# Optimization experiments

Measured on AMD Instinct MI355X. Metric: run time of the kernel, lower is better.

The kernel has to match this reference:

```python
import jax, jax.numpy as jnp
import numpy as np

MU = 0.5
SIGMA = 0.5


def relu_zono(M, c, slopes):
    """Zonotope ReLU relaxation with learnable slopes.
    M: [k, n] error-term magnitudes, c: [n] center, slopes: [n].
    Returns (M', c') where M' has n extra rows (new error terms; rows for
    non-crossing neurons are exactly zero, matching the torch math up to
    zero-row padding so shapes stay static under jit).
    """
    abs_vals = jnp.sum(jnp.abs(M), axis=0)            # [n]
    lx = c - abs_vals
    ux = c + abs_vals
    basic = ux / (ux - lx)                            # denom = 2*abs_vals > 0 a.s.
    zero_mask = ux <= 0
    cross_mask = (ux > 0) & (lx <= 0)
    in_range = (slopes >= 0) & (slopes <= basic)
    left = cross_mask & in_range
    right = cross_mask & jnp.logical_not(in_range)
    mag = jnp.where(left, (1.0 - slopes) * ux * 0.5,
          jnp.where(right, -slopes * lx * 0.5, 0.0))  # [n] new error magnitudes
    col_scale = jnp.where(zero_mask, 0.0, jnp.where(cross_mask, slopes, 1.0))
    M = M * col_scale[None, :]
    c = jnp.where(zero_mask, 0.0, jnp.where(cross_mask, slopes * c + mag, c))
    M = jnp.concatenate([M, jnp.diag(mag)], axis=0)   # one new row per neuron
    return M, c


def zono_forward(M, c, slopes1, slopes2, W1, b1, W2, b2, W3, b3):
    # Normalization layer: center normalized, magnitudes divided by sigma
    c = (c - MU) / SIGMA
    M = M / SIGMA
    # Linear 1 (bias only applies to center, matching F.linear(M, W) w/o bias)
    M = M @ W1.T
    c = c @ W1.T + b1
    M, c = relu_zono(M, c, slopes1)
    # Linear 2
    M = M @ W2.T
    c = c @ W2.T + b2
    M, c = relu_zono(M, c, slopes2)
    # Linear 3 (logits)
    M = M @ W3.T
    c = c @ W3.T + b3
    return M, c


def setup_inputs() -> dict:
    key = jax.random.key(0)
    ks = jax.random.split(key, 10)
    d_in, h, d_out = 3072, 4096, 10
    magnitude_matrix = jax.random.normal(ks[0], (d_in, d_in), jnp.float32) * 0.001
    center = jax.random.normal(ks[1], (d_in,), jnp.float32)
    slopes1 = jax.random.uniform(ks[2], (h,), jnp.float32)
    slopes2 = jax.random.uniform(ks[3], (h,), jnp.float32)
    W1 = jax.random.normal(ks[4], (h, d_in), jnp.float32) / np.sqrt(d_in)
    b1 = jax.random.normal(ks[5], (h,), jnp.float32) * 0.1
    W2 = jax.random.normal(ks[6], (h, h), jnp.float32) / np.sqrt(h)
    b2 = jax.random.normal(ks[7], (h,), jnp.float32) * 0.1
    W3 = jax.random.normal(ks[8], (d_out, h), jnp.float32) / np.sqrt(h)
    b3 = jax.random.normal(ks[9], (d_out,), jnp.float32) * 0.1
    return {"magnitude_matrix": magnitude_matrix, "center": center,
            "slopes1": slopes1, "slopes2": slopes2,
            "W1": W1, "b1": b1, "W2": W2, "b2": b2, "W3": W3, "b3": b3}


def reference(magnitude_matrix, center, slopes1, slopes2, W1, b1, W2, b2, W3, b3):
    return zono_forward(magnitude_matrix, center, slopes1, slopes2,
                        W1, b1, W2, b2, W3, b3)
```

## Files before the change

kernel.cpp:

```cpp
#include <hip/hip_runtime.h>
#include <cstddef>
#include <cstdint>

#define DIN 3072
#define DH  4096
#define DOUT 10

typedef float4 f4;
typedef __attribute__((ext_vector_type(4))) int   int32x4;
typedef __attribute__((ext_vector_type(8))) char  charx8;

#define R_A1 0.013f
#define R_W1 0.117275f
#define R_T1 0.013f
#define R_W2 0.1015625f

__device__ __forceinline__ short f2bf(float x) {
    unsigned u = __builtin_bit_cast(unsigned, x);
    u = (u + 0x7FFFu + ((u >> 16) & 1u)) >> 16;
    return (short)u;
}
__device__ __forceinline__ float bf2f(short x) {
    unsigned u = ((unsigned)(unsigned short)x) << 16;
    return __builtin_bit_cast(float, u);
}
__device__ __forceinline__ char q8(float x, float s) {
    float r = rintf(x * s);
    r = fminf(127.f, fmaxf(-127.f, r));
    return (char)(int)r;
}

__device__ __forceinline__ void gload_lds16(const char* g, char* l) {
    __builtin_amdgcn_global_load_lds(
        (const __attribute__((address_space(1))) unsigned int*)g,
        (__attribute__((address_space(3))) unsigned int*)l,
        16, 0, 0);
}

__global__ void init_kernel(const float* __restrict__ c, float* __restrict__ cn,
                            float* __restrict__ abs1, float* __restrict__ out) {
    int i = blockIdx.x * 256 + threadIdx.x;
    abs1[i] = 0.f;
    if (i < DIN) cn[i] = (c[i] - 0.5f) * 2.0f;
    size_t base = (size_t)(DIN + i) * DOUT;
#pragma unroll
    for (int o = 0; o < DOUT; ++o) out[base + o] = 0.f;
}

__global__ void quant8_kernel(const float* __restrict__ in, char* __restrict__ out,
                              float s, int n8) {
    int i = blockIdx.x * 256 + threadIdx.x;
    if (i >= n8) return;
    const f4* p = (const f4*)(in + (size_t)i * 8);
    f4 v0 = p[0], v1 = p[1];
    charx8 o;
    o[0] = q8(v0.x, s); o[1] = q8(v0.y, s); o[2] = q8(v0.z, s); o[3] = q8(v0.w, s);
    o[4] = q8(v1.x, s); o[5] = q8(v1.y, s); o[6] = q8(v1.z, s); o[7] = q8(v1.w, s);
    *(charx8*)(out + (size_t)i * 8) = o;
}

__global__ __launch_bounds__(384)
void quant_w1_fused(const float* __restrict__ W1, const float* __restrict__ cn,
                    char* __restrict__ W1q, float* __restrict__ c1acc, float s)
{
    int j = blockIdx.x, t = threadIdx.x;
    int lane = t & 63, wave = t >> 6;
    const float* row = W1 + (size_t)j * DIN;
    size_t base = (size_t)t * 8;
    f4 v0 = *(const f4*)&row[base], v1 = *(const f4*)&row[base + 4];
    f4 u0 = *(const f4*)&cn[base],  u1 = *(const f4*)&cn[base + 4];
    charx8 o;
    o[0] = q8(v0.x, s); o[1] = q8(v0.y, s); o[2] = q8(v0.z, s); o[3] = q8(v0.w, s);
    o[4] = q8(v1.x, s); o[5] = q8(v1.y, s); o[6] = q8(v1.z, s); o[7] = q8(v1.w, s);
    *(charx8*)&W1q[(size_t)j * DIN + base] = o;
    float acc = v0.x*u0.x + v0.y*u0.y + v0.z*u0.z + v0.w*u0.w
              + v1.x*u1.x + v1.y*u1.y + v1.z*u1.z + v1.w*u1.w;
#pragma unroll
    for (int m = 32; m >= 1; m >>= 1) acc += __shfl_xor(acc, m, 64);
    __shared__ float red[6];
    if (lane == 0) red[wave] = acc;
    __syncthreads();
    if (t == 0) c1acc[j] = red[0] + red[1] + red[2] + red[3] + red[4] + red[5];
}

__global__ __launch_bounds__(512)
void quant_w2_fused(const float* __restrict__ W2, const float* __restrict__ cs1,
                    const float* __restrict__ c1p, const float* __restrict__ mag1,
                    char* __restrict__ W2q, float* __restrict__ c2acc,
                    float* __restrict__ abs2, float s)
{
    int j = blockIdx.x, t = threadIdx.x;
    int lane = t & 63, wave = t >> 6;
    const float* row = W2 + (size_t)j * DH;
    size_t base = (size_t)t * 8;
    f4 v0 = *(const f4*)&row[base], v1 = *(const f4*)&row[base + 4];
    f4 s0 = *(const f4*)&cs1[base], s1 = *(const f4*)&cs1[base + 4];
    f4 p0 = *(const f4*)&c1p[base], p1 = *(const f4*)&c1p[base + 4];
    f4 m0 = *(const f4*)&mag1[base], m1 = *(const f4*)&mag1[base + 4];
    charx8 o;
    o[0] = q8(v0.x * s0.x, s); o[1] = q8(v0.y * s0.y, s);
    o[2] = q8(v0.z * s0.z, s); o[3] = q8(v0.w * s0.w, s);
    o[4] = q8(v1.x * s1.x, s); o[5] = q8(v1.y * s1.y, s);
    o[6] = q8(v1.z * s1.z, s); o[7] = q8(v1.w * s1.w, s);
    *(charx8*)&W2q[(size_t)j * DH + base] = o;
    float a = p0.x*v0.x + p0.y*v0.y + p0.z*v0.z + p0.w*v0.w
            + p1.x*v1.x + p1.y*v1.y + p1.z*v1.z + p1.w*v1.w;
    float b = m0.x*fabsf(v0.x) + m0.y*fabsf(v0.y) + m0.z*fabsf(v0.z) + m0.w*fabsf(v0.w)
            + m1.x*fabsf(v1.x) + m1.y*fabsf(v1.y) + m1.z*fabsf(v1.z) + m1.w*fabsf(v1.w);
#pragma unroll
    for (int m = 32; m >= 1; m >>= 1) {
        a += __shfl_xor(a, m, 64);
        b += __shfl_xor(b, m, 64);
    }
    __shared__ float reda[8], redb[8];
    if (lane == 0) { reda[wave] = a; redb[wave] = b; }
    __syncthreads();
    if (t == 0) {
        float sa = 0.f, sb = 0.f;
#pragma unroll
        for (int w = 0; w < 8; ++w) { sa += reda[w]; sb += redb[w]; }
        c2acc[j] = sa; abs2[j] = sb;
    }
}

template<int OUT8>
__global__ __launch_bounds__(512, 2)
void gemm_i8nt(const char* __restrict__ A, const char* __restrict__ B,
               void* __restrict__ Cout, float* __restrict__ absout,
               int M, int N, int K, float ds, float oscale)
{
    __shared__ char lds[2][4][16384];

    const int tid  = threadIdx.x;
    const int lane = tid & 63, wid = tid >> 6;
    const int wm = wid >> 2, wn = wid & 3;
    const int fr = lane & 15, fh = lane >> 4;

    const int gx = gridDim.x;
    const int nwg = gx * gridDim.y;
    const int orig = blockIdx.y * gx + blockIdx.x;
    const int swz = (orig & 7) * (nwg >> 3) + (orig >> 3);
    const int bx = swz % gx, by = swz / gx;
    const int row0 = by * 256, col0 = bx * 256;

    const char* Apan = A + (size_t)row0 * K;
    const char* Bpan = B + (size_t)col0 * K;

    const int s0 = wid * 64 + lane;
    const int r0 = s0 >> 3;  const int c0 = ((s0 & 7) ^ (r0 & 7)) * 16;
    const int s1 = s0 + 512;
    const int r1 = s1 >> 3;  const int c1 = ((s1 & 7) ^ (r1 & 7)) * 16;
    const int d0 = wid * 1024;
    const int d1 = 8192 + wid * 1024;

    const int xr = fr & 7;
    const int ch0 = ((0 + fh) ^ xr) * 16;
    const int ch1 = ((4 + fh) ^ xr) * 16;
    const int brow = (wn & 1) * 64;

#define STAGE(bi, part, u) do {                                                   \
    const char* _s = ((part) < 2 ? Apan : Bpan)                                   \
                     + (size_t)(((part) & 1) * 128) * K + (size_t)(u) * 128;      \
    char* _d = &lds[bi][part][0];                                                 \
    gload_lds16(_s + (size_t)r0 * K + c0, _d + d0);                               \
    gload_lds16(_s + (size_t)r1 * K + c1, _d + d1);                               \
} while (0)

    int32x4 acc[8][4];
#pragma unroll
    for (int i = 0; i < 8; ++i)
#pragma unroll
        for (int j = 0; j < 4; ++j) acc[i][j] = (int32x4){0, 0, 0, 0};

    int32x4 a[4][2], b0[2][2], b1[2][2];
    const int NT = K >> 7;

#define KSTEP(CUR, NXT, SA, AU, SB, BU, LAST)                                      \
  {                                                                                \
    const char* Al = &lds[CUR][wm][0];                                             \
    const char* Bl = &lds[CUR][2 + (wn >> 1)][0];                                  \
                                                                \
    _Pragma("unroll") for (int f = 0; f < 4; ++f) {                                \
      a[f][0] = *(const int32x4*)&Al[(f * 16 + fr) * 128 + ch0];                   \
      a[f][1] = *(const int32x4*)&Al[(f * 16 + fr) * 128 + ch1];                   \
    }                                                                              \
    _Pragma("unroll") for (int nf = 0; nf < 2; ++nf) {                             \
      b0[nf][0] = *(const int32x4*)&Bl[(brow + nf * 16 + fr) * 128 + ch0];         \
      b0[nf][1] = *(const int32x4*)&Bl[(brow + nf * 16 + fr) * 128 + ch1];         \
    }                                                                              \
    if (SA) STAGE(NXT, 0, AU);                                                     \
    __builtin_amdgcn_s_barrier();                                                  \
    asm volatile("s_waitcnt lgkmcnt(0)" ::: "memory");                             \
    __builtin_amdgcn_sched_barrier(0);                                             \
    __builtin_amdgcn_s_setprio(1);                                                 \
    _Pragma("unroll") for (int f = 0; f < 4; ++f)                                  \
      _Pragma("unroll") for (int nf = 0; nf < 2; ++nf) {                           \
        acc[f][nf] = __builtin_amdgcn_mfma_i32_16x16x64_i8(a[f][0], b0[nf][0], acc[f][nf], 0, 0, 0); \
        acc[f][nf] = __builtin_amdgcn_mfma_i32_16x16x64_i8(a[f][1], b0[nf][1], acc[f][nf], 0, 0, 0); \
      }                                                                            \
    __builtin_amdgcn_s_setprio(0);                                                 \
    __builtin_amdgcn_s_barrier();                                                  \
                                                                \
    _Pragma("unroll") for (int nf = 0; nf < 2; ++nf) {                             \
      b1[nf][0] = *(const int32x4*)&Bl[(brow + 32 + nf * 16 + fr) * 128 + ch0];    \
      b1[nf][1] = *(const int32x4*)&Bl[(brow + 32 + nf * 16 + fr) * 128 + ch1];    \
    }                                                                              \
    if (SA) STAGE(NXT, 1, AU);                                                     \
    __builtin_amdgcn_s_barrier();                                                  \
    asm volatile("s_waitcnt lgkmcnt(0)" ::: "memory");                             \
    __builtin_amdgcn_sched_barrier(0);                                             \
    __builtin_amdgcn_s_setprio(1);                                                 \
    _Pragma("unroll") for (int f = 0; f < 4; ++f)                                  \
      _Pragma("unroll") for (int nf = 0; nf < 2; ++nf) {                           \
        acc[f][2+nf] = __builtin_amdgcn_mfma_i32_16x16x64_i8(a[f][0], b1[nf][0], acc[f][2+nf], 0, 0, 0); \
        acc[f][2+nf] = __builtin_amdgcn_mfma_i32_16x16x64_i8(a[f][1], b1[nf][1], acc[f][2+nf], 0, 0, 0); \
      }                                                                            \
    __builtin_amdgcn_s_setprio(0);                                                 \
    __builtin_amdgcn_s_barrier();                                                  \
                                                                \
    _Pragma("unroll") for (int f = 0; f < 4; ++f) {                                \
      a[f][0] = *(const int32x4*)&Al[((f + 4) * 16 + fr) * 128 + ch0];             \
      a[f][1] = *(const int32x4*)&Al[((f + 4) * 16 + fr) * 128 + ch1];             \
    }                                                                              \
    if (SB) STAGE(CUR, 2, BU);                                                     \
    __builtin_amdgcn_s_barrier();                                                  \
    asm volatile("s_waitcnt lgkmcnt(0)" ::: "memory");                             \
    __builtin_amdgcn_sched_barrier(0);                                             \
    __builtin_amdgcn_s_setprio(1);                                                 \
    _Pragma("unroll") for (int f = 0; f < 4; ++f)                                  \
      _Pragma("unroll") for (int nf = 0; nf < 2; ++nf) {                           \
        acc[4+f][2+nf] = __builtin_amdgcn_mfma_i32_16x16x64_i8(a[f][0], b1[nf][0], acc[4+f][2+nf], 0, 0, 0); \
        acc[4+f][2+nf] = __builtin_amdgcn_mfma_i32_16x16x64_i8(a[f][1], b1[nf][1], acc[4+f][2+nf], 0, 0, 0); \
      }                                                                            \
    __builtin_amdgcn_s_setprio(0);                                                 \
    __builtin_amdgcn_s_barrier();                                                  \
                                                 \
    if (SB) STAGE(CUR, 3, BU);                                                     \
    __builtin_amdgcn_s_setprio(1);                                                 \
    _Pragma("unroll") for (int f = 0; f < 4; ++f)                                  \
      _Pragma("unroll") for (int nf = 0; nf < 2; ++nf) {                           \
        acc[4+f][nf] = __builtin_amdgcn_mfma_i32_16x16x64_i8(a[f][0], b0[nf][0], acc[4+f][nf], 0, 0, 0); \
        acc[4+f][nf] = __builtin_amdgcn_mfma_i32_16x16x64_i8(a[f][1], b0[nf][1], acc[4+f][nf], 0, 0, 0); \
      }                                                                            \
    __builtin_amdgcn_s_setprio(0);                                                 \
    if (LAST) { asm volatile("s_waitcnt vmcnt(0)" ::: "memory"); }                 \
    else      { asm volatile("s_waitcnt vmcnt(4)" ::: "memory"); }                 \
    __builtin_amdgcn_s_barrier();                                                  \
  }

    STAGE(0, 0, 0); STAGE(0, 1, 0); STAGE(0, 2, 0); STAGE(0, 3, 0);
    STAGE(1, 2, 1); STAGE(1, 3, 1);
    asm volatile("s_waitcnt vmcnt(4)" ::: "memory");
    __builtin_amdgcn_s_barrier();

    int u = 0;
    for (; u + 3 < NT; u += 2) {
        KSTEP(0, 1, 1, u + 1, 1, u + 2, 0)
        KSTEP(1, 0, 1, u + 2, 1, u + 3, 0)
    }
    KSTEP(0, 1, 1, NT - 1, 0, 0, 1)
    KSTEP(1, 0, 0, 0, 0, 0, 1)
#undef KSTEP
#undef STAGE

    const int cr = row0 + wm * 128 + fh * 4;
    const int cc = col0 + wn * 64 + fr;
    float csum[4];
#pragma unroll
    for (int nf = 0; nf < 4; ++nf) {
        float s = 0.f;
#pragma unroll
        for (int f = 0; f < 8; ++f)
#pragma unroll
            for (int j = 0; j < 4; ++j) {
                float v = (float)acc[f][nf][j] * ds;
                s += fabsf(v);
                size_t idx = (size_t)(cr + f * 16 + j) * N + cc + nf * 16;
                if (OUT8) ((char*)Cout)[idx] = q8(v, oscale);
                else      ((short*)Cout)[idx] = f2bf(v);
            }
        s += __shfl_xor(s, 16, 64);
        s += __shfl_xor(s, 32, 64);
        csum[nf] = s;
    }
    if (fh == 0) {
#pragma unroll
        for (int nf = 0; nf < 4; ++nf)
            atomicAdd(&absout[col0 + wn * 64 + nf * 16 + fr], csum[nf]);
    }
}

__global__ void relu_params_kernel(const float* __restrict__ absv, const float* __restrict__ cacc,
                                   const float* __restrict__ bias, const float* __restrict__ slopes,
                                   float* __restrict__ mag, float* __restrict__ cs,
                                   float* __restrict__ cp, int n)
{
    int j = blockIdx.x * 256 + threadIdx.x;
    if (j >= n) return;
    float a = absv[j];
    float cin = cacc[j] + bias[j];
    float s = slopes[j];
    float lx = cin - a, ux = cin + a;
    float basic = ux / (ux - lx);
    bool zero  = (ux <= 0.f);
    bool cross = (ux > 0.f) && (lx <= 0.f);
    bool inr   = (s >= 0.f) && (s <= basic);
    float mg = cross ? (inr ? (1.f - s) * ux * 0.5f : -s * lx * 0.5f) : 0.f;
    mag[j] = mg;
    cs[j]  = zero ? 0.f : (cross ? s : 1.f);
    cp[j]  = zero ? 0.f : (cross ? s * cin + mg : cin);
}

__global__ void relu2_fused(const float* __restrict__ absv, const float* __restrict__ cacc,
                            const float* __restrict__ bias, const float* __restrict__ slopes,
                            const float* __restrict__ W3,
                            float* __restrict__ cp, float* __restrict__ V,
                            float* __restrict__ out)
{
    int j = blockIdx.x * 256 + threadIdx.x;
    if (j >= DH) return;
    float a = absv[j];
    float cin = cacc[j] + bias[j];
    float s = slopes[j];
    float lx = cin - a, ux = cin + a;
    float basic = ux / (ux - lx);
    bool zero  = (ux <= 0.f);
    bool cross = (ux > 0.f) && (lx <= 0.f);
    bool inr   = (s >= 0.f) && (s <= basic);
    float mg = cross ? (inr ? (1.f - s) * ux * 0.5f : -s * lx * 0.5f) : 0.f;
    float csv = zero ? 0.f : (cross ? s : 1.f);
    cp[j] = zero ? 0.f : (cross ? s * cin + mg : cin);
    size_t base = (size_t)(DIN + DH + j) * DOUT;
#pragma unroll
    for (int o = 0; o < DOUT; ++o) {
        float w = W3[(size_t)o * DH + j];
        V[j * DOUT + o] = csv * w;
        out[base + o] = mg * w;
    }
}

__global__ __launch_bounds__(256)
void out_fused(const short* __restrict__ T2, const float* __restrict__ V,
               const float* __restrict__ W2, const float* __restrict__ mag1,
               const float* __restrict__ c2p, const float* __restrict__ W3,
               const float* __restrict__ b3, float* __restrict__ out)
{
    int b = blockIdx.x, tid = threadIdx.x;
    int lane = tid & 63, wave = tid >> 6;
    __shared__ float red[4][DOUT];

    if (b < DIN / 4) {
        int r = b * 4 + wave;
        const short* trow = T2 + (size_t)r * DH;
        float acc[DOUT];
#pragma unroll
        for (int o = 0; o < DOUT; ++o) acc[o] = 0.f;
        for (int j = lane; j < DH; j += 64) {
            float t = bf2f(trow[j]);
            const float* vr = V + j * DOUT;
#pragma unroll
            for (int o = 0; o < DOUT; ++o) acc[o] += t * vr[o];
        }
#pragma unroll
        for (int o = 0; o < DOUT; ++o)
            for (int m = 32; m >= 1; m >>= 1) acc[o] += __shfl_xor(acc[o], m, 64);
        if (lane == 0) {
#pragma unroll
            for (int o = 0; o < DOUT; ++o) out[(size_t)r * DOUT + o] = acc[o];
        }
    } else if (b < DIN / 4 + 256) {
        int bb = b - DIN / 4;
        int i = (bb & 15) * 256 + tid;
        int j0 = (bb >> 4) * 256;
        float acc[DOUT];
#pragma unroll
        for (int o = 0; o < DOUT; ++o) acc[o] = 0.f;
        for (int j = j0; j < j0 + 256; ++j) {
            float w = W2[(size_t)j * DH + i];
            const float* vr = V + j * DOUT;
#pragma unroll
            for (int o = 0; o < DOUT; ++o) acc[o] += w * vr[o];
        }
        float m = mag1[i];
        size_t base = (size_t)(DIN + i) * DOUT;
#pragma unroll
        for (int o = 0; o < DOUT; ++o) atomicAdd(&out[base + o], m * acc[o]);
    } else {
        float acc[DOUT];
#pragma unroll
        for (int o = 0; o < DOUT; ++o) acc[o] = 0.f;
        for (int j = tid; j < DH; j += 256) {
            float cv = c2p[j];
#pragma unroll
            for (int o = 0; o < DOUT; ++o) acc[o] += cv * W3[(size_t)o * DH + j];
        }
#pragma unroll
        for (int o = 0; o < DOUT; ++o)
            for (int m = 32; m >= 1; m >>= 1) acc[o] += __shfl_xor(acc[o], m, 64);
        if (lane == 0)
#pragma unroll
            for (int o = 0; o < DOUT; ++o) red[wave][o] = acc[o];
        __syncthreads();
        if (tid < DOUT) {
            float s = red[0][tid] + red[1][tid] + red[2][tid] + red[3][tid] + b3[tid];
            out[(size_t)(DIN + DH + DH) * DOUT + tid] = s;
        }
    }
}

extern "C" void kernel_launch(void* const* d_in, const int* in_sizes, int n_in,
                              void* d_out, int out_size, void* d_ws, size_t ws_size,
                              hipStream_t stream)
{
    const float* Mm = (const float*)d_in[0];
    const float* c  = (const float*)d_in[1];
    const float* s1 = (const float*)d_in[2];
    const float* s2 = (const float*)d_in[3];
    const float* W1 = (const float*)d_in[4];
    const float* b1 = (const float*)d_in[5];
    const float* W2 = (const float*)d_in[6];
    const float* b2 = (const float*)d_in[7];
    const float* W3 = (const float*)d_in[8];
    const float* b3 = (const float*)d_in[9];
    float* out = (float*)d_out;

    char* w = (char*)d_ws;
    short* T2b  = (short*)w;                                  w += (size_t)DIN * DH * 2;
    float* V    = (float*)w;                                  w += (size_t)DH * DOUT * 4;
    float* abs1 = (float*)w;                                  w += DH * 4;
    float* abs2 = (float*)w;                                  w += DH * 4;
    float* mag1 = (float*)w;                                  w += DH * 4;
    float* cs1  = (float*)w;                                  w += DH * 4;
    float* c1p  = (float*)w;                                  w += DH * 4;
    float* c1acc= (float*)w;                                  w += DH * 4;
    float* c2acc= (float*)w;                                  w += DH * 4;
    float* c2p  = (float*)w;                                  w += DH * 4;
    float* cn   = (float*)w;                                  w += DIN * 4;
    char*  Aq   = w;                                          w += (size_t)DIN * DIN;
    char*  Wq   = w;                                          w += (size_t)DH * DH;
    char*  T1q  = w;                                          w += (size_t)DIN * DH;

    const float invA1 = 127.f / R_A1;
    const float invW1 = 127.f / R_W1;
    const float invT1 = 127.f / R_T1;
    const float invW2 = 127.f / R_W2;
    const float ds1 = (R_A1 / 127.f) * (R_W1 / 127.f);
    const float ds2 = (R_T1 / 127.f) * (R_W2 / 127.f);

    init_kernel<<<16, 256, 0, stream>>>(c, cn, abs1, out);

    quant8_kernel<<<DIN * DIN / 8 / 256, 256, 0, stream>>>(Mm, Aq, 2.f * invA1, DIN * DIN / 8);
    quant_w1_fused<<<DH, 384, 0, stream>>>(W1, cn, Wq, c1acc, invW1);

    gemm_i8nt<1><<<dim3(DH / 256, DIN / 256), 512, 0, stream>>>(
        Aq, Wq, T1q, abs1, DIN, DH, DIN, ds1, invT1);
    relu_params_kernel<<<16, 256, 0, stream>>>(abs1, c1acc, b1, s1, mag1, cs1, c1p, DH);

    quant_w2_fused<<<DH, 512, 0, stream>>>(W2, cs1, c1p, mag1, Wq, c2acc, abs2, invW2);
    gemm_i8nt<0><<<dim3(DH / 256, DIN / 256), 512, 0, stream>>>(
        T1q, Wq, T2b, abs2, DIN, DH, DH, ds2, 0.f);
    relu2_fused<<<16, 256, 0, stream>>>(abs2, c2acc, b2, s2, W3, c2p, V, out);

    out_fused<<<DIN / 4 + 256 + 1, 256, 0, stream>>>(T2b, V, W2, mag1, c2p, W3, b3, out);
}
```

Before: 203.1 us.

## Fuse prep kernels, use 192-row GEMM tiles, read int8 W2 in output stage

Merges the init, A-quantisation and W1-quantisation kernels into one launch and folds the centre normalisation into the W1 dot product. Both int8 GEMMs switch from 256x256 to 192x256 tiles, which gives 16x16=256 workgroups instead of 192 and so fills more CUs, at the cost of less reuse per tile. The final stage now reads the already quantised, slope-scaled int8 W2 with a per-column correction factor instead of the fp32 W2, cutting its memory traffic but adding a division by the column scale.

```diff
diff --git a/kernel.cpp b/kernel.cpp
--- a/kernel.cpp
+++ b/kernel.cpp
@@ -37,50 +37,52 @@
         16, 0, 0);
 }
 
-__global__ void init_kernel(const float* __restrict__ c, float* __restrict__ cn,
-                            float* __restrict__ abs1, float* __restrict__ out) {
-    int i = blockIdx.x * 256 + threadIdx.x;
-    abs1[i] = 0.f;
-    if (i < DIN) cn[i] = (c[i] - 0.5f) * 2.0f;
-    size_t base = (size_t)(DIN + i) * DOUT;
-#pragma unroll
-    for (int o = 0; o < DOUT; ++o) out[base + o] = 0.f;
-}
-
-__global__ void quant8_kernel(const float* __restrict__ in, char* __restrict__ out,
-                              float s, int n8) {
-    int i = blockIdx.x * 256 + threadIdx.x;
-    if (i >= n8) return;
-    const f4* p = (const f4*)(in + (size_t)i * 8);
-    f4 v0 = p[0], v1 = p[1];
-    charx8 o;
-    o[0] = q8(v0.x, s); o[1] = q8(v0.y, s); o[2] = q8(v0.z, s); o[3] = q8(v0.w, s);
-    o[4] = q8(v1.x, s); o[5] = q8(v1.y, s); o[6] = q8(v1.z, s); o[7] = q8(v1.w, s);
-    *(charx8*)(out + (size_t)i * 8) = o;
-}
-
 __global__ __launch_bounds__(384)
-void quant_w1_fused(const float* __restrict__ W1, const float* __restrict__ cn,
-                    char* __restrict__ W1q, float* __restrict__ c1acc, float s)
-{
-    int j = blockIdx.x, t = threadIdx.x;
-    int lane = t & 63, wave = t >> 6;
-    const float* row = W1 + (size_t)j * DIN;
-    size_t base = (size_t)t * 8;
-    f4 v0 = *(const f4*)&row[base], v1 = *(const f4*)&row[base + 4];
-    f4 u0 = *(const f4*)&cn[base],  u1 = *(const f4*)&cn[base + 4];
-    charx8 o;
-    o[0] = q8(v0.x, s); o[1] = q8(v0.y, s); o[2] = q8(v0.z, s); o[3] = q8(v0.w, s);
-    o[4] = q8(v1.x, s); o[5] = q8(v1.y, s); o[6] = q8(v1.z, s); o[7] = q8(v1.w, s);
-    *(charx8*)&W1q[(size_t)j * DIN + base] = o;
-    float acc = v0.x*u0.x + v0.y*u0.y + v0.z*u0.z + v0.w*u0.w
-              + v1.x*u1.x + v1.y*u1.y + v1.z*u1.z + v1.w*u1.w;
-#pragma unroll
-    for (int m = 32; m >= 1; m >>= 1) acc += __shfl_xor(acc, m, 64);
-    __shared__ float red[6];
-    if (lane == 0) red[wave] = acc;
-    __syncthreads();
-    if (t == 0) c1acc[j] = red[0] + red[1] + red[2] + red[3] + red[4] + red[5];
+void prep1_kernel(const float* __restrict__ Mm, const float* __restrict__ W1,
+                  const float* __restrict__ c,
+                  char* __restrict__ Aq, char* __restrict__ W1q,
+                  float* __restrict__ c1acc, float* __restrict__ abs1,
+                  float* __restrict__ out, float sA, float sW)
+{
+    int b = blockIdx.x, t = threadIdx.x;
+    if (b < 3072) {
+        size_t i = ((size_t)b * 384 + t) * 8;
+        const f4* p = (const f4*)(Mm + i);
+        f4 v0 = p[0], v1 = p[1];
+        charx8 o;
+        o[0] = q8(v0.x, sA); o[1] = q8(v0.y, sA); o[2] = q8(v0.z, sA); o[3] = q8(v0.w, sA);
+        o[4] = q8(v1.x, sA); o[5] = q8(v1.y, sA); o[6] = q8(v1.z, sA); o[7] = q8(v1.w, sA);
+        *(charx8*)(Aq + i) = o;
+    } else if (b < 7168) {
+        int j = b - 3072;
+        int lane = t & 63, wave = t >> 6;
+        const float* row = W1 + (size_t)j * DIN;
+        size_t base = (size_t)t * 8;
+        f4 v0 = *(const f4*)&row[base], v1 = *(const f4*)&row[base + 4];
+        f4 u0 = *(const f4*)&c[base],   u1 = *(const f4*)&c[base + 4];
+        charx8 o;
+        o[0] = q8(v0.x, sW); o[1] = q8(v0.y, sW); o[2] = q8(v0.z, sW); o[3] = q8(v0.w, sW);
+        o[4] = q8(v1.x, sW); o[5] = q8(v1.y, sW); o[6] = q8(v1.z, sW); o[7] = q8(v1.w, sW);
+        *(charx8*)&W1q[(size_t)j * DIN + base] = o;
+        float acc = v0.x*((u0.x-0.5f)*2.f) + v0.y*((u0.y-0.5f)*2.f)
+                  + v0.z*((u0.z-0.5f)*2.f) + v0.w*((u0.w-0.5f)*2.f)
+                  + v1.x*((u1.x-0.5f)*2.f) + v1.y*((u1.y-0.5f)*2.f)
+                  + v1.z*((u1.z-0.5f)*2.f) + v1.w*((u1.w-0.5f)*2.f);
+#pragma unroll
+        for (int m = 32; m >= 1; m >>= 1) acc += __shfl_xor(acc, m, 64);
+        __shared__ float red[6];
+        if (lane == 0) red[wave] = acc;
+        __syncthreads();
+        if (t == 0) c1acc[j] = red[0] + red[1] + red[2] + red[3] + red[4] + red[5];
+    } else {
+        int idx = (b - 7168) * 384 + t;
+        if (idx < DH) {
+            abs1[idx] = 0.f;
+            size_t base = (size_t)(DIN + idx) * DOUT;
+#pragma unroll
+            for (int o = 0; o < DOUT; ++o) out[base + o] = 0.f;
+        }
+    }
 }
 
 __global__ __launch_bounds__(512)
@@ -129,7 +131,7 @@
                void* __restrict__ Cout, float* __restrict__ absout,
                int M, int N, int K, float ds, float oscale)
 {
-    __shared__ char lds[2][4][16384];
+    __shared__ char lds[2][57344];
 
     const int tid  = threadIdx.x;
     const int lane = tid & 63, wid = tid >> 6;
@@ -141,46 +143,55 @@
     const int orig = blockIdx.y * gx + blockIdx.x;
     const int swz = (orig & 7) * (nwg >> 3) + (orig >> 3);
     const int bx = swz % gx, by = swz / gx;
-    const int row0 = by * 256, col0 = bx * 256;
+    const int row0 = by * 192, col0 = bx * 256;
 
     const char* Apan = A + (size_t)row0 * K;
     const char* Bpan = B + (size_t)col0 * K;
 
     const int s0 = wid * 64 + lane;
-    const int r0 = s0 >> 3;  const int c0 = ((s0 & 7) ^ (r0 & 7)) * 16;
+    const int rA0 = s0 >> 3;          const int cA0 = ((s0 & 7) ^ (rA0 & 7)) * 16;
     const int s1 = s0 + 512;
-    const int r1 = s1 >> 3;  const int c1 = ((s1 & 7) ^ (r1 & 7)) * 16;
+    const int rA1 = s1 >> 3;          const int cA1 = ((s1 & 7) ^ (rA1 & 7)) * 16;
+    const int s2 = s0 + 1024;
+    const int rA2 = s2 >> 3;          const int cA2 = ((s2 & 7) ^ (rA2 & 7)) * 16;
     const int d0 = wid * 1024;
     const int d1 = 8192 + wid * 1024;
+    const int d2 = 16384 + wid * 1024;
 
     const int xr = fr & 7;
     const int ch0 = ((0 + fh) ^ xr) * 16;
     const int ch1 = ((4 + fh) ^ xr) * 16;
     const int brow = (wn & 1) * 64;
 
-#define STAGE(bi, part, u) do {                                                   \
-    const char* _s = ((part) < 2 ? Apan : Bpan)                                   \
-                     + (size_t)(((part) & 1) * 128) * K + (size_t)(u) * 128;      \
-    char* _d = &lds[bi][part][0];                                                 \
-    gload_lds16(_s + (size_t)r0 * K + c0, _d + d0);                               \
-    gload_lds16(_s + (size_t)r1 * K + c1, _d + d1);                               \
+#define STAGE_A(bi, u) do {                                                       \
+    const char* _s = Apan + (size_t)(u) * 128;                                    \
+    char* _d = lds[bi];                                                           \
+    gload_lds16(_s + (size_t)rA0 * K + cA0, _d + d0);                             \
+    gload_lds16(_s + (size_t)rA1 * K + cA1, _d + d1);                             \
+    gload_lds16(_s + (size_t)rA2 * K + cA2, _d + d2);                             \
 } while (0)
-
-    int32x4 acc[8][4];
-#pragma unroll
-    for (int i = 0; i < 8; ++i)
+#define STAGE_B(bi, half, u) do {                                                 \
+    const char* _s = Bpan + (size_t)((half) * 128) * K + (size_t)(u) * 128;       \
+    char* _d = lds[bi] + 24576 + (half) * 16384;                                  \
+    gload_lds16(_s + (size_t)rA0 * K + cA0, _d + d0);                             \
+    gload_lds16(_s + (size_t)rA1 * K + cA1, _d + d1);                             \
+} while (0)
+
+    int32x4 acc[6][4];
+#pragma unroll
+    for (int i = 0; i < 6; ++i)
 #pragma unroll
         for (int j = 0; j < 4; ++j) acc[i][j] = (int32x4){0, 0, 0, 0};
 
-    int32x4 a[4][2], b0[2][2], b1[2][2];
+    int32x4 a[3][2], b0[2][2], b1[2][2];
     const int NT = K >> 7;
 
 #define KSTEP(CUR, NXT, SA, AU, SB, BU, LAST)                                      \
   {                                                                                \
-    const char* Al = &lds[CUR][wm][0];                                             \
-    const char* Bl = &lds[CUR][2 + (wn >> 1)][0];                                  \
+    const char* Al = lds[CUR] + wm * 12288;                                        \
+    const char* Bl = lds[CUR] + 24576 + (wn >> 1) * 16384;                         \
                                                                 \
-    _Pragma("unroll") for (int f = 0; f < 4; ++f) {                                \
+    _Pragma("unroll") for (int f = 0; f < 3; ++f) {                                \
       a[f][0] = *(const int32x4*)&Al[(f * 16 + fr) * 128 + ch0];                   \
       a[f][1] = *(const int32x4*)&Al[(f * 16 + fr) * 128 + ch1];                   \
     }                                                                              \
@@ -188,12 +199,12 @@
       b0[nf][0] = *(const int32x4*)&Bl[(brow + nf * 16 + fr) * 128 + ch0];         \
       b0[nf][1] = *(const int32x4*)&Bl[(brow + nf * 16 + fr) * 128 + ch1];         \
     }                                                                              \
-    if (SA) STAGE(NXT, 0, AU);                                                     \
+    if (SA) STAGE_A(NXT, AU);                                                      \
     __builtin_amdgcn_s_barrier();                                                  \
     asm volatile("s_waitcnt lgkmcnt(0)" ::: "memory");                             \
     __builtin_amdgcn_sched_barrier(0);                                             \
     __builtin_amdgcn_s_setprio(1);                                                 \
-    _Pragma("unroll") for (int f = 0; f < 4; ++f)                                  \
+    _Pragma("unroll") for (int f = 0; f < 3; ++f)                                  \
       _Pragma("unroll") for (int nf = 0; nf < 2; ++nf) {                           \
         acc[f][nf] = __builtin_amdgcn_mfma_i32_16x16x64_i8(a[f][0], b0[nf][0], acc[f][nf], 0, 0, 0); \
         acc[f][nf] = __builtin_amdgcn_mfma_i32_16x16x64_i8(a[f][1], b0[nf][1], acc[f][nf], 0, 0, 0); \
@@ -205,12 +216,11 @@
       b1[nf][0] = *(const int32x4*)&Bl[(brow + 32 + nf * 16 + fr) * 128 + ch0];    \
       b1[nf][1] = *(const int32x4*)&Bl[(brow + 32 + nf * 16 + fr) * 128 + ch1];    \
     }                                                                              \
-    if (SA) STAGE(NXT, 1, AU);                                                     \
     __builtin_amdgcn_s_barrier();                                                  \
     asm volatile("s_waitcnt lgkmcnt(0)" ::: "memory");                             \
     __builtin_amdgcn_sched_barrier(0);                                             \
     __builtin_amdgcn_s_setprio(1);                                                 \
-    _Pragma("unroll") for (int f = 0; f < 4; ++f)                                  \
+    _Pragma("unroll") for (int f = 0; f < 3; ++f)                                  \
       _Pragma("unroll") for (int nf = 0; nf < 2; ++nf) {                           \
         acc[f][2+nf] = __builtin_amdgcn_mfma_i32_16x16x64_i8(a[f][0], b1[nf][0], acc[f][2+nf], 0, 0, 0); \
         acc[f][2+nf] = __builtin_amdgcn_mfma_i32_16x16x64_i8(a[f][1], b1[nf][1], acc[f][2+nf], 0, 0, 0); \
@@ -218,29 +228,29 @@
     __builtin_amdgcn_s_setprio(0);                                                 \
     __builtin_amdgcn_s_barrier();                                                  \
                                                                 \
-    _Pragma("unroll") for (int f = 0; f < 4; ++f) {                                \
-      a[f][0] = *(const int32x4*)&Al[((f + 4) * 16 + fr) * 128 + ch0];             \
-      a[f][1] = *(const int32x4*)&Al[((f + 4) * 16 + fr) * 128 + ch1];             \
+    _Pragma("unroll") for (int f = 0; f < 3; ++f) {                                \
+      a[f][0] = *(const int32x4*)&Al[((f + 3) * 16 + fr) * 128 + ch0];             \
+      a[f][1] = *(const int32x4*)&Al[((f + 3) * 16 + fr) * 128 + ch1];             \
     }                                                                              \
-    if (SB) STAGE(CUR, 2, BU);                                                     \
+    if (SB) STAGE_B(CUR, 0, BU);                                                   \
     __builtin_amdgcn_s_barrier();                                                  \
     asm volatile("s_waitcnt lgkmcnt(0)" ::: "memory");                             \
     __builtin_amdgcn_sched_barrier(0);                                             \
     __builtin_amdgcn_s_setprio(1);                                                 \
-    _Pragma("unroll") for (int f = 0; f < 4; ++f)                                  \
+    _Pragma("unroll") for (int f = 0; f < 3; ++f)                                  \
       _Pragma("unroll") for (int nf = 0; nf < 2; ++nf) {                           \
-        acc[4+f][2+nf] = __builtin_amdgcn_mfma_i32_16x16x64_i8(a[f][0], b1[nf][0], acc[4+f][2+nf], 0, 0, 0); \
-        acc[4+f][2+nf] = __builtin_amdgcn_mfma_i32_16x16x64_i8(a[f][1], b1[nf][1], acc[4+f][2+nf], 0, 0, 0); \
+        acc[3+f][2+nf] = __builtin_amdgcn_mfma_i32_16x16x64_i8(a[f][0], b1[nf][0], acc[3+f][2+nf], 0, 0, 0); \
+        acc[3+f][2+nf] = __builtin_amdgcn_mfma_i32_16x16x64_i8(a[f][1], b1[nf][1], acc[3+f][2+nf], 0, 0, 0); \
       }                                                                            \
     __builtin_amdgcn_s_setprio(0);                                                 \
     __builtin_amdgcn_s_barrier();                                                  \
                                                  \
-    if (SB) STAGE(CUR, 3, BU);                                                     \
+    if (SB) STAGE_B(CUR, 1, BU);                                                   \
     __builtin_amdgcn_s_setprio(1);                                                 \
-    _Pragma("unroll") for (int f = 0; f < 4; ++f)                                  \
+    _Pragma("unroll") for (int f = 0; f < 3; ++f)                                  \
       _Pragma("unroll") for (int nf = 0; nf < 2; ++nf) {                           \
-        acc[4+f][nf] = __builtin_amdgcn_mfma_i32_16x16x64_i8(a[f][0], b0[nf][0], acc[4+f][nf], 0, 0, 0); \
-        acc[4+f][nf] = __builtin_amdgcn_mfma_i32_16x16x64_i8(a[f][1], b0[nf][1], acc[4+f][nf], 0, 0, 0); \
+        acc[3+f][nf] = __builtin_amdgcn_mfma_i32_16x16x64_i8(a[f][0], b0[nf][0], acc[3+f][nf], 0, 0, 0); \
+        acc[3+f][nf] = __builtin_amdgcn_mfma_i32_16x16x64_i8(a[f][1], b0[nf][1], acc[3+f][nf], 0, 0, 0); \
       }                                                                            \
     __builtin_amdgcn_s_setprio(0);                                                 \
     if (LAST) { asm volatile("s_waitcnt vmcnt(0)" ::: "memory"); }                 \
@@ -248,8 +258,8 @@
     __builtin_amdgcn_s_barrier();                                                  \
   }
 
-    STAGE(0, 0, 0); STAGE(0, 1, 0); STAGE(0, 2, 0); STAGE(0, 3, 0);
-    STAGE(1, 2, 1); STAGE(1, 3, 1);
+    STAGE_A(0, 0); STAGE_B(0, 0, 0); STAGE_B(0, 1, 0);
+    STAGE_B(1, 0, 1); STAGE_B(1, 1, 1);
     asm volatile("s_waitcnt vmcnt(4)" ::: "memory");
     __builtin_amdgcn_s_barrier();
 
@@ -261,16 +271,17 @@
     KSTEP(0, 1, 1, NT - 1, 0, 0, 1)
     KSTEP(1, 0, 0, 0, 0, 0, 1)
 #undef KSTEP
-#undef STAGE
-
-    const int cr = row0 + wm * 128 + fh * 4;
+#undef STAGE_A
+#undef STAGE_B
+
+    const int cr = row0 + wm * 96 + fh * 4;
     const int cc = col0 + wn * 64 + fr;
     float csum[4];
 #pragma unroll
     for (int nf = 0; nf < 4; ++nf) {
         float s = 0.f;
 #pragma unroll
-        for (int f = 0; f < 8; ++f)
+        for (int f = 0; f < 6; ++f)
 #pragma unroll
             for (int j = 0; j < 4; ++j) {
                 float v = (float)acc[f][nf][j] * ds;
@@ -293,7 +304,8 @@
 __global__ void relu_params_kernel(const float* __restrict__ absv, const float* __restrict__ cacc,
                                    const float* __restrict__ bias, const float* __restrict__ slopes,
                                    float* __restrict__ mag, float* __restrict__ cs,
-                                   float* __restrict__ cp, int n)
+                                   float* __restrict__ cp, float* __restrict__ fac,
+                                   float fscale, int n)
 {
     int j = blockIdx.x * 256 + threadIdx.x;
     if (j >= n) return;
@@ -306,9 +318,11 @@
     bool cross = (ux > 0.f) && (lx <= 0.f);
     bool inr   = (s >= 0.f) && (s <= basic);
     float mg = cross ? (inr ? (1.f - s) * ux * 0.5f : -s * lx * 0.5f) : 0.f;
+    float csv = zero ? 0.f : (cross ? s : 1.f);
     mag[j] = mg;
-    cs[j]  = zero ? 0.f : (cross ? s : 1.f);
+    cs[j]  = csv;
     cp[j]  = zero ? 0.f : (cross ? s * cin + mg : cin);
+    fac[j] = (csv != 0.f) ? (mg / csv) * fscale : 0.f;
 }
 
 __global__ void relu2_fused(const float* __restrict__ absv, const float* __restrict__ cacc,
@@ -341,7 +355,7 @@
 
 __global__ __launch_bounds__(256)
 void out_fused(const short* __restrict__ T2, const float* __restrict__ V,
-               const float* __restrict__ W2, const float* __restrict__ mag1,
+               const char* __restrict__ W2q, const float* __restrict__ fac1,
                const float* __restrict__ c2p, const float* __restrict__ W3,
                const float* __restrict__ b3, float* __restrict__ out)
 {
@@ -376,12 +390,12 @@
 #pragma unroll
         for (int o = 0; o < DOUT; ++o) acc[o] = 0.f;
         for (int j = j0; j < j0 + 256; ++j) {
-            float w = W2[(size_t)j * DH + i];
+            float w = (float)W2q[(size_t)j * DH + i];
             const float* vr = V + j * DOUT;
 #pragma unroll
             for (int o = 0; o < DOUT; ++o) acc[o] += w * vr[o];
         }
-        float m = mag1[i];
+        float m = fac1[i];
         size_t base = (size_t)(DIN + i) * DOUT;
 #pragma unroll
         for (int o = 0; o < DOUT; ++o) atomicAdd(&out[base + o], m * acc[o]);
@@ -435,7 +449,7 @@
     float* c1acc= (float*)w;                                  w += DH * 4;
     float* c2acc= (float*)w;                                  w += DH * 4;
     float* c2p  = (float*)w;                                  w += DH * 4;
-    float* cn   = (float*)w;                                  w += DIN * 4;
+    float* fac1 = (float*)w;                                  w += DH * 4;
     char*  Aq   = w;                                          w += (size_t)DIN * DIN;
     char*  Wq   = w;                                          w += (size_t)DH * DH;
     char*  T1q  = w;                                          w += (size_t)DIN * DH;
@@ -447,19 +461,18 @@
     const float ds1 = (R_A1 / 127.f) * (R_W1 / 127.f);
     const float ds2 = (R_T1 / 127.f) * (R_W2 / 127.f);
 
-    init_kernel<<<16, 256, 0, stream>>>(c, cn, abs1, out);
-
-    quant8_kernel<<<DIN * DIN / 8 / 256, 256, 0, stream>>>(Mm, Aq, 2.f * invA1, DIN * DIN / 8);
-    quant_w1_fused<<<DH, 384, 0, stream>>>(W1, cn, Wq, c1acc, invW1);
-
-    gemm_i8nt<1><<<dim3(DH / 256, DIN / 256), 512, 0, stream>>>(
+    prep1_kernel<<<3072 + 4096 + 16, 384, 0, stream>>>(
+        Mm, W1, c, Aq, Wq, c1acc, abs1, out, 2.f * invA1, invW1);
+
+    gemm_i8nt<1><<<dim3(DH / 256, DIN / 192), 512, 0, stream>>>(
         Aq, Wq, T1q, abs1, DIN, DH, DIN, ds1, invT1);
-    relu_params_kernel<<<16, 256, 0, stream>>>(abs1, c1acc, b1, s1, mag1, cs1, c1p, DH);
+    relu_params_kernel<<<16, 256, 0, stream>>>(
+        abs1, c1acc, b1, s1, mag1, cs1, c1p, fac1, R_W2 / 127.f, DH);
 
     quant_w2_fused<<<DH, 512, 0, stream>>>(W2, cs1, c1p, mag1, Wq, c2acc, abs2, invW2);
-    gemm_i8nt<0><<<dim3(DH / 256, DIN / 256), 512, 0, stream>>>(
+    gemm_i8nt<0><<<dim3(DH / 256, DIN / 192), 512, 0, stream>>>(
         T1q, Wq, T2b, abs2, DIN, DH, DH, ds2, 0.f);
     relu2_fused<<<16, 256, 0, stream>>>(abs2, c2acc, b2, s2, W3, c2p, V, out);
 
-    out_fused<<<DIN / 4 + 256 + 1, 256, 0, stream>>>(T2b, V, W2, mag1, c2p, W3, b3, out);
-}
+    out_fused<<<DIN / 4 + 256 + 1, 256, 0, stream>>>(T2b, V, Wq, fac1, c2p, W3, b3, out);
+}
```

Result: faster. 180.7 us (-11.1%).
